# Kernel optimization log

Measured on AMD Instinct MI355X. Metric: run time of the kernel, lower is better.

The kernel has to match this reference:

```python
import jax, jax.numpy as jnp
import numpy as np

N = 4096          # leng_doc (number of tokens)
D_S = 70          # DEP_EMB_DIM + 2*BI_LSTM_PHASE_1_OUTPUT_DIM = 10 + 60

def setup_inputs() -> dict:
    key = jax.random.key(0)
    k1, k2 = jax.random.split(key)
    adj = jax.random.uniform(k1, (N, N, 2), dtype=jnp.float32)   # unweighted adjacency, 2 edge directions/channels
    s = jax.random.normal(k2, (N, D_S), dtype=jnp.float32)       # per-node edge-representation s
    return {"adj": adj, "s": s}

def reference(adj, s):
    # Faithful to CalculateHLayer-style math (CalculateSLayer analog):
    #   s_in[j,d]  = sum_i sum_k adj[i,j,k] * s[i,d]
    #   s_out[i,d] = sum_j sum_k adj[i,j,k] * s[j,d]
    # Sum over the channel axis k first, then contract the node axis with a GEMM
    # instead of materializing the (N,N,2,D) broadcast intermediate.
    a = adj.sum(axis=2)                 # (N, N)
    s_in = jnp.einsum('ij,id->jd', a, s)   # reduce over source nodes -> (N, D)
    s_out = jnp.einsum('ij,jd->id', a, s)  # reduce over target nodes -> (N, D)
    return (s_in, s_out)
```

## Files before the change

kernel.cpp:

```cpp
#include <hip/hip_runtime.h>


#define N    4096
#define D    70
#define DP   80
#define TILE 128
#define NT_D 5
#define NPART 32
#define ATP  132

typedef short short8  __attribute__((ext_vector_type(8)));
typedef short short4v __attribute__((ext_vector_type(4)));
typedef float f32x4   __attribute__((ext_vector_type(4)));

__device__ __forceinline__ unsigned short f2bf(float f) {
    unsigned u = __builtin_bit_cast(unsigned, f);
    u += 0x7FFFu + ((u >> 16) & 1u);
    return (unsigned short)(u >> 16);
}
__device__ __forceinline__ float bf2f(unsigned short h) {
    unsigned u = (unsigned)h << 16;
    return __builtin_bit_cast(float, u);
}
__device__ __forceinline__ short8 ld_b64x2(const unsigned short* p) {
    short4v lo = *(const short4v*)p;
    short4v hi = *(const short4v*)(p + 4);
    return __builtin_shufflevector(lo, hi, 0, 1, 2, 3, 4, 5, 6, 7);
}

__global__ __launch_bounds__(256) void build_sT(const float* __restrict__ s,
                                                unsigned short* __restrict__ sT) {
    __shared__ unsigned short tile[DP][264];
    const int t  = threadIdx.x;
    const int n0 = blockIdx.x * 256;
    #pragma unroll
    for (int d = 0; d < D; ++d)
        tile[d][t] = f2bf(s[(size_t)(n0 + t) * D + d]);
    __syncthreads();
    #pragma unroll
    for (int d = 0; d < DP; ++d) {
        unsigned short v = (d < D) ? tile[d][t] : (unsigned short)0;
        sT[(size_t)d * N + n0 + t] = v;
    }
}

template<bool USE_WS>
__global__ __launch_bounds__(512, 4) void fused_slayer(
    const float* __restrict__ adj,
    const unsigned short* __restrict__ sT,
    void* __restrict__ p_in_,
    void* __restrict__ p_out_)
{
    unsigned short* wi = (unsigned short*)p_in_;
    unsigned short* wo = (unsigned short*)p_out_;
    float* oi = (float*)p_in_;
    float* oo = (float*)p_out_;

    __shared__ __align__(16) unsigned short a_row[TILE][40];
    __shared__ __align__(16) unsigned short aTt[32][ATP];
    __shared__ __align__(16) unsigned short sTi[DP][136];
    __shared__ __align__(16) unsigned short sTj[DP][136];

    const int t    = threadIdx.x;
    const int lane = t & 63;
    const int w    = t >> 6;
    const int l16  = lane & 15;
    const int q    = lane >> 4;

    const int I0 = blockIdx.y * TILE;
    const int J0 = blockIdx.x * TILE;

    {
        const int c  = t & 15;
        const int rr = t >> 4;
        #pragma unroll
        for (int p = 0; p < 3; ++p) {
            int d = rr + 32 * p;
            if (d < DP) {
                uint4 vi = *(const uint4*)(sT + (size_t)d * N + I0 + 8 * c);
                uint4 vj = *(const uint4*)(sT + (size_t)d * N + J0 + 8 * c);
                *(uint4*)&sTi[d][8 * c] = vi;
                *(uint4*)&sTj[d][8 * c] = vj;
            }
        }
    }

    const f32x4 zero = {0.0f, 0.0f, 0.0f, 0.0f};
    f32x4 acc1[NT_D];
    #pragma unroll
    for (int nt = 0; nt < NT_D; ++nt) acc1[nt] = zero;

    const int slot_mt = w & 1;
    const int slot_nt = w >> 1;
    const bool extra  = (w < 2);

    const int jp = t & 15;
    const int ir = t >> 4;

    float4 v[4];
    #pragma unroll
    for (int it = 0; it < 4; ++it) {
        int i = 32 * it + ir;
        v[it] = *(const float4*)(adj + (size_t)(I0 + i) * (2 * N)
                                     + (size_t)(J0 + 2 * jp) * 2);
    }

    #pragma unroll
    for (int jc = 0; jc < 4; ++jc) {
        __syncthreads();

        #pragma unroll
        for (int it = 0; it < 4; ++it) {
            int i = 32 * it + ir;
            unsigned short b0 = f2bf(v[it].x + v[it].y);
            unsigned short b1 = f2bf(v[it].z + v[it].w);
            *(unsigned int*)&a_row[i][2 * jp] =
                (unsigned int)b0 | ((unsigned int)b1 << 16);
            aTt[2 * jp][i]     = b0;
            aTt[2 * jp + 1][i] = b1;
        }
        __syncthreads();

        if (jc < 3) {
            #pragma unroll
            for (int it = 0; it < 4; ++it) {
                int i = 32 * it + ir;
                v[it] = *(const float4*)(adj + (size_t)(I0 + i) * (2 * N)
                                             + (size_t)(J0 + 32 * (jc + 1) + 2 * jp) * 2);
            }
        }

        {
            short8 af = *(const short8*)&a_row[16 * w + l16][8 * q];
            #pragma unroll
            for (int nt = 0; nt < NT_D; ++nt) {
                short8 bf = *(const short8*)&sTj[16 * nt + l16][32 * jc + 8 * q];
                acc1[nt] = __builtin_amdgcn_mfma_f32_16x16x32_bf16(af, bf, acc1[nt], 0, 0, 0);
            }
        }

        {
            f32x4 acc2 = zero;
            #pragma unroll
            for (int ks = 0; ks < 4; ++ks) {
                short8 af = ld_b64x2(&aTt[16 * slot_mt + l16][32 * ks + 8 * q]);
                short8 bf = *(const short8*)&sTi[16 * slot_nt + l16][32 * ks + 8 * q];
                acc2 = __builtin_amdgcn_mfma_f32_16x16x32_bf16(af, bf, acc2, 0, 0, 0);
            }
            int d = 16 * slot_nt + l16;
            #pragma unroll
            for (int r = 0; r < 4; ++r) {
                int gj = J0 + 32 * jc + 16 * slot_mt + 4 * q + r;
                if (USE_WS) {
                    wi[((size_t)blockIdx.y * N + gj) * DP + d] = f2bf(acc2[r]);
                } else if (d < D) {
                    atomicAdd(&oi[(size_t)gj * D + d], acc2[r]);
                }
            }
            if (extra) {
                f32x4 acc3 = zero;
                #pragma unroll
                for (int ks = 0; ks < 4; ++ks) {
                    short8 af = ld_b64x2(&aTt[16 * w + l16][32 * ks + 8 * q]);
                    short8 bf = *(const short8*)&sTi[64 + l16][32 * ks + 8 * q];
                    acc3 = __builtin_amdgcn_mfma_f32_16x16x32_bf16(af, bf, acc3, 0, 0, 0);
                }
                int d2 = 64 + l16;
                #pragma unroll
                for (int r = 0; r < 4; ++r) {
                    int gj = J0 + 32 * jc + 16 * w + 4 * q + r;
                    if (USE_WS) {
                        wi[((size_t)blockIdx.y * N + gj) * DP + d2] = f2bf(acc3[r]);
                    } else if (d2 < D) {
                        atomicAdd(&oi[(size_t)gj * D + d2], acc3[r]);
                    }
                }
            }
        }
    }

    #pragma unroll
    for (int nt = 0; nt < NT_D; ++nt) {
        int d = 16 * nt + l16;
        #pragma unroll
        for (int r = 0; r < 4; ++r) {
            int gi = I0 + 16 * w + 4 * q + r;
            if (USE_WS) {
                wo[((size_t)blockIdx.x * N + gi) * DP + d] = f2bf(acc1[nt][r]);
            } else if (d < D) {
                atomicAdd(&oo[(size_t)gi * D + d], acc1[nt][r]);
            }
        }
    }
}

__global__ __launch_bounds__(128) void reduce_partials(
    const unsigned short* __restrict__ ws, float* __restrict__ out) {
    const int idx   = blockIdx.x * 128 + threadIdx.x;
    const int which = idx / (N * (DP / 8));
    const int rem   = idx % (N * (DP / 8));
    const int j     = rem / (DP / 8);
    const int g     = rem % (DP / 8);

    const unsigned short* base = ws + (size_t)which * ((size_t)NPART * N * DP)
                                    + (size_t)j * DP + 8 * g;
    float acc[8];
    #pragma unroll
    for (int e = 0; e < 8; ++e) acc[e] = 0.0f;
    #pragma unroll 8
    for (int p = 0; p < NPART; ++p) {
        short8 v = *(const short8*)(base + (size_t)p * N * DP);
        #pragma unroll
        for (int e = 0; e < 8; ++e)
            acc[e] += bf2f((unsigned short)v[e]);
    }

    float* o = out + (size_t)which * (N * D) + (size_t)j * D;
    #pragma unroll
    for (int e = 0; e < 8; ++e) {
        int d = 8 * g + e;
        if (d < D) o[d] = acc[e];
    }
}

extern "C" void kernel_launch(void* const* d_in, const int* in_sizes, int n_in,
                              void* d_out, int out_size, void* d_ws, size_t ws_size,
                              hipStream_t stream) {
    const float* adj = (const float*)d_in[0];
    const float* s   = (const float*)d_in[1];
    float* out = (float*)d_out;

    unsigned short* sT = (unsigned short*)d_ws;
    const size_t ST_BYTES = (size_t)DP * N * sizeof(unsigned short);
    unsigned short* ws_part = (unsigned short*)((char*)d_ws + ST_BYTES);
    const size_t PART_ELEMS = (size_t)NPART * N * DP;
    const size_t NEED = ST_BYTES + 2 * PART_ELEMS * sizeof(unsigned short);

    build_sT<<<dim3(N / 256), dim3(256), 0, stream>>>(s, sT);

    if (ws_size >= NEED) {
        fused_slayer<true><<<dim3(N / TILE, N / TILE), dim3(512), 0, stream>>>(
            adj, sT, ws_part , ws_part + PART_ELEMS );
        reduce_partials<<<dim3(2 * N * (DP / 8) / 128), dim3(128), 0, stream>>>(
            ws_part, out);
    } else {
        hipMemsetAsync(d_out, 0, (size_t)2 * N * D * sizeof(float), stream);
        fused_slayer<false><<<dim3(N / TILE, N / TILE), dim3(512), 0, stream>>>(
            adj, sT, out , out + (size_t)N * D );
    }
}
```

Before: 212.1 us.

## Fuse partial reduction into main kernel via last-block counters, double-buffer adjacency tiles

```diff
diff --git a/kernel.cpp b/kernel.cpp
--- a/kernel.cpp
+++ b/kernel.cpp
@@ -8,6 +8,7 @@
 #define NT_D 5
 #define NPART 32
 #define ATP  132
+#define SJP  136
 
 typedef short short8  __attribute__((ext_vector_type(8)));
 typedef short short4v __attribute__((ext_vector_type(4)));
@@ -48,51 +49,56 @@
 __global__ __launch_bounds__(512, 4) void fused_slayer(
     const float* __restrict__ adj,
     const unsigned short* __restrict__ sT,
-    void* __restrict__ p_in_,
-    void* __restrict__ p_out_)
+    unsigned short* __restrict__ wsi,
+    unsigned short* __restrict__ wso,
+    unsigned int*   __restrict__ cnt,
+    float* __restrict__ out)
 {
-    unsigned short* wi = (unsigned short*)p_in_;
-    unsigned short* wo = (unsigned short*)p_out_;
-    float* oi = (float*)p_in_;
-    float* oo = (float*)p_out_;
-
-    __shared__ __align__(16) unsigned short a_row[TILE][40];
-    __shared__ __align__(16) unsigned short aTt[32][ATP];
-    __shared__ __align__(16) unsigned short sTi[DP][136];
-    __shared__ __align__(16) unsigned short sTj[DP][136];
+    __shared__ __align__(16) unsigned short a_row[2][TILE][40];
+    __shared__ __align__(16) unsigned short aTt[2][32][ATP];
+    __shared__ __align__(16) unsigned short sTj[DP][SJP];
+    __shared__ int flag_in, flag_out;
 
     const int t    = threadIdx.x;
     const int lane = t & 63;
     const int w    = t >> 6;
     const int l16  = lane & 15;
     const int q    = lane >> 4;
-
-    const int I0 = blockIdx.y * TILE;
-    const int J0 = blockIdx.x * TILE;
-
-    {
-        const int c  = t & 15;
-        const int rr = t >> 4;
-        #pragma unroll
-        for (int p = 0; p < 3; ++p) {
-            int d = rr + 32 * p;
-            if (d < DP) {
-                uint4 vi = *(const uint4*)(sT + (size_t)d * N + I0 + 8 * c);
-                uint4 vj = *(const uint4*)(sT + (size_t)d * N + J0 + 8 * c);
-                *(uint4*)&sTi[d][8 * c] = vi;
-                *(uint4*)&sTj[d][8 * c] = vj;
-            }
-        }
-    }
-
-    const f32x4 zero = {0.0f, 0.0f, 0.0f, 0.0f};
-    f32x4 acc1[NT_D];
-    #pragma unroll
-    for (int nt = 0; nt < NT_D; ++nt) acc1[nt] = zero;
+    const int bx   = blockIdx.x;
+    const int by   = blockIdx.y;
+    const int I0   = by * TILE;
+    const int J0   = bx * TILE;
+
+    #pragma unroll
+    for (int p = 0; p < 3; ++p) {
+        int ii = t + 512 * p;
+        if (ii < DP * 16) {
+            int d = ii >> 4, c = ii & 15;
+            *(uint4*)&sTj[d][8 * c] = *(const uint4*)(sT + (size_t)d * N + J0 + 8 * c);
+        }
+    }
 
     const int slot_mt = w & 1;
     const int slot_nt = w >> 1;
     const bool extra  = (w < 2);
+    short8 bfi[4], bfe[4];
+    {
+        const int d = 16 * slot_nt + l16;
+        #pragma unroll
+        for (int ks = 0; ks < 4; ++ks)
+            bfi[ks] = *(const short8*)(sT + (size_t)d * N + I0 + 32 * ks + 8 * q);
+        if (extra) {
+            const int d2 = 64 + l16;
+            #pragma unroll
+            for (int ks = 0; ks < 4; ++ks)
+                bfe[ks] = *(const short8*)(sT + (size_t)d2 * N + I0 + 32 * ks + 8 * q);
+        }
+    }
+
+    const f32x4 zero = {0.0f, 0.0f, 0.0f, 0.0f};
+    f32x4 acc1[NT_D];
+    #pragma unroll
+    for (int nt = 0; nt < NT_D; ++nt) acc1[nt] = zero;
 
     const int jp = t & 15;
     const int ir = t >> 4;
@@ -107,17 +113,17 @@
 
     #pragma unroll
     for (int jc = 0; jc < 4; ++jc) {
-        __syncthreads();
+        const int b = jc & 1;
 
         #pragma unroll
         for (int it = 0; it < 4; ++it) {
             int i = 32 * it + ir;
             unsigned short b0 = f2bf(v[it].x + v[it].y);
             unsigned short b1 = f2bf(v[it].z + v[it].w);
-            *(unsigned int*)&a_row[i][2 * jp] =
+            *(unsigned int*)&a_row[b][i][2 * jp] =
                 (unsigned int)b0 | ((unsigned int)b1 << 16);
-            aTt[2 * jp][i]     = b0;
-            aTt[2 * jp + 1][i] = b1;
+            aTt[b][2 * jp][i]     = b0;
+            aTt[b][2 * jp + 1][i] = b1;
         }
         __syncthreads();
 
@@ -131,7 +137,7 @@
         }
 
         {
-            short8 af = *(const short8*)&a_row[16 * w + l16][8 * q];
+            short8 af = *(const short8*)&a_row[b][16 * w + l16][8 * q];
             #pragma unroll
             for (int nt = 0; nt < NT_D; ++nt) {
                 short8 bf = *(const short8*)&sTj[16 * nt + l16][32 * jc + 8 * q];
@@ -143,36 +149,34 @@
             f32x4 acc2 = zero;
             #pragma unroll
             for (int ks = 0; ks < 4; ++ks) {
-                short8 af = ld_b64x2(&aTt[16 * slot_mt + l16][32 * ks + 8 * q]);
-                short8 bf = *(const short8*)&sTi[16 * slot_nt + l16][32 * ks + 8 * q];
-                acc2 = __builtin_amdgcn_mfma_f32_16x16x32_bf16(af, bf, acc2, 0, 0, 0);
-            }
-            int d = 16 * slot_nt + l16;
+                short8 af2 = ld_b64x2(&aTt[b][16 * slot_mt + l16][32 * ks + 8 * q]);
+                acc2 = __builtin_amdgcn_mfma_f32_16x16x32_bf16(af2, bfi[ks], acc2, 0, 0, 0);
+            }
+            const int d = 16 * slot_nt + l16;
             #pragma unroll
             for (int r = 0; r < 4; ++r) {
                 int gj = J0 + 32 * jc + 16 * slot_mt + 4 * q + r;
                 if (USE_WS) {
-                    wi[((size_t)blockIdx.y * N + gj) * DP + d] = f2bf(acc2[r]);
+                    wsi[((size_t)by * N + gj) * DP + d] = f2bf(acc2[r]);
                 } else if (d < D) {
-                    atomicAdd(&oi[(size_t)gj * D + d], acc2[r]);
+                    atomicAdd(&out[(size_t)gj * D + d], acc2[r]);
                 }
             }
             if (extra) {
                 f32x4 acc3 = zero;
                 #pragma unroll
                 for (int ks = 0; ks < 4; ++ks) {
-                    short8 af = ld_b64x2(&aTt[16 * w + l16][32 * ks + 8 * q]);
-                    short8 bf = *(const short8*)&sTi[64 + l16][32 * ks + 8 * q];
-                    acc3 = __builtin_amdgcn_mfma_f32_16x16x32_bf16(af, bf, acc3, 0, 0, 0);
+                    short8 af3 = ld_b64x2(&aTt[b][16 * w + l16][32 * ks + 8 * q]);
+                    acc3 = __builtin_amdgcn_mfma_f32_16x16x32_bf16(af3, bfe[ks], acc3, 0, 0, 0);
                 }
-                int d2 = 64 + l16;
+                const int d2 = 64 + l16;
                 #pragma unroll
                 for (int r = 0; r < 4; ++r) {
                     int gj = J0 + 32 * jc + 16 * w + 4 * q + r;
                     if (USE_WS) {
-                        wi[((size_t)blockIdx.y * N + gj) * DP + d2] = f2bf(acc3[r]);
+                        wsi[((size_t)by * N + gj) * DP + d2] = f2bf(acc3[r]);
                     } else if (d2 < D) {
-                        atomicAdd(&oi[(size_t)gj * D + d2], acc3[r]);
+                        atomicAdd(&out[(size_t)gj * D + d2], acc3[r]);
                     }
                 }
             }
@@ -181,45 +185,71 @@
 
     #pragma unroll
     for (int nt = 0; nt < NT_D; ++nt) {
-        int d = 16 * nt + l16;
+        const int d = 16 * nt + l16;
         #pragma unroll
         for (int r = 0; r < 4; ++r) {
             int gi = I0 + 16 * w + 4 * q + r;
             if (USE_WS) {
-                wo[((size_t)blockIdx.x * N + gi) * DP + d] = f2bf(acc1[nt][r]);
+                wso[((size_t)bx * N + gi) * DP + d] = f2bf(acc1[nt][r]);
             } else if (d < D) {
-                atomicAdd(&oo[(size_t)gi * D + d], acc1[nt][r]);
-            }
-        }
-    }
-}
-
-__global__ __launch_bounds__(128) void reduce_partials(
-    const unsigned short* __restrict__ ws, float* __restrict__ out) {
-    const int idx   = blockIdx.x * 128 + threadIdx.x;
-    const int which = idx / (N * (DP / 8));
-    const int rem   = idx % (N * (DP / 8));
-    const int j     = rem / (DP / 8);
-    const int g     = rem % (DP / 8);
-
-    const unsigned short* base = ws + (size_t)which * ((size_t)NPART * N * DP)
-                                    + (size_t)j * DP + 8 * g;
-    float acc[8];
-    #pragma unroll
-    for (int e = 0; e < 8; ++e) acc[e] = 0.0f;
-    #pragma unroll 8
-    for (int p = 0; p < NPART; ++p) {
-        short8 v = *(const short8*)(base + (size_t)p * N * DP);
-        #pragma unroll
-        for (int e = 0; e < 8; ++e)
-            acc[e] += bf2f((unsigned short)v[e]);
-    }
-
-    float* o = out + (size_t)which * (N * D) + (size_t)j * D;
-    #pragma unroll
-    for (int e = 0; e < 8; ++e) {
-        int d = 8 * g + e;
-        if (d < D) o[d] = acc[e];
+                atomicAdd(&out[(size_t)N * D + (size_t)gi * D + d], acc1[nt][r]);
+            }
+        }
+    }
+
+    if (!USE_WS) return;
+
+    __threadfence();
+    __syncthreads();
+    if (t == 0) {
+        flag_in  = (atomicAdd(&cnt[bx],      1u) == NPART - 1);
+        flag_out = (atomicAdd(&cnt[32 + by], 1u) == NPART - 1);
+    }
+    __syncthreads();
+
+    if (flag_in) {
+        __threadfence();
+        for (int task = t; task < TILE * (DP / 8); task += 512) {
+            const int jl = task / (DP / 8);
+            const int g  = task % (DP / 8);
+            const int gj = J0 + jl;
+            float acc[8];
+            #pragma unroll
+            for (int e = 0; e < 8; ++e) acc[e] = 0.0f;
+            #pragma unroll 8
+            for (int p = 0; p < NPART; ++p) {
+                short8 vv = *(const short8*)(wsi + ((size_t)p * N + gj) * DP + 8 * g);
+                #pragma unroll
+                for (int e = 0; e < 8; ++e) acc[e] += bf2f((unsigned short)vv[e]);
+            }
+            #pragma unroll
+            for (int e = 0; e < 8; ++e) {
+                int d = 8 * g + e;
+                if (d < D) out[(size_t)gj * D + d] = acc[e];
+            }
+        }
+    }
+    if (flag_out) {
+        __threadfence();
+        for (int task = t; task < TILE * (DP / 8); task += 512) {
+            const int il = task / (DP / 8);
+            const int g  = task % (DP / 8);
+            const int gi = I0 + il;
+            float acc[8];
+            #pragma unroll
+            for (int e = 0; e < 8; ++e) acc[e] = 0.0f;
+            #pragma unroll 8
+            for (int p = 0; p < NPART; ++p) {
+                short8 vv = *(const short8*)(wso + ((size_t)p * N + gi) * DP + 8 * g);
+                #pragma unroll
+                for (int e = 0; e < 8; ++e) acc[e] += bf2f((unsigned short)vv[e]);
+            }
+            #pragma unroll
+            for (int e = 0; e < 8; ++e) {
+                int d = 8 * g + e;
+                if (d < D) out[(size_t)N * D + (size_t)gi * D + d] = acc[e];
+            }
+        }
     }
 }
 
@@ -231,21 +261,22 @@
     float* out = (float*)d_out;
 
     unsigned short* sT = (unsigned short*)d_ws;
-    const size_t ST_BYTES = (size_t)DP * N * sizeof(unsigned short);
-    unsigned short* ws_part = (unsigned short*)((char*)d_ws + ST_BYTES);
+    const size_t ST_BYTES   = (size_t)DP * N * sizeof(unsigned short);
+    unsigned int*   cnt     = (unsigned int*)((char*)d_ws + ST_BYTES);
+    unsigned short* ws_part = (unsigned short*)((char*)d_ws + ST_BYTES + 256);
     const size_t PART_ELEMS = (size_t)NPART * N * DP;
-    const size_t NEED = ST_BYTES + 2 * PART_ELEMS * sizeof(unsigned short);
+    const size_t NEED = ST_BYTES + 256
+                      + 2 * PART_ELEMS * sizeof(unsigned short);
 
     build_sT<<<dim3(N / 256), dim3(256), 0, stream>>>(s, sT);
 
     if (ws_size >= NEED) {
+        hipMemsetAsync(cnt, 0, 256, stream);
         fused_slayer<true><<<dim3(N / TILE, N / TILE), dim3(512), 0, stream>>>(
-            adj, sT, ws_part , ws_part + PART_ELEMS );
-        reduce_partials<<<dim3(2 * N * (DP / 8) / 128), dim3(128), 0, stream>>>(
-            ws_part, out);
+            adj, sT, ws_part, ws_part + PART_ELEMS, cnt, out);
     } else {
         hipMemsetAsync(d_out, 0, (size_t)2 * N * D * sizeof(float), stream);
         fused_slayer<false><<<dim3(N / TILE, N / TILE), dim3(512), 0, stream>>>(
-            adj, sT, out , out + (size_t)N * D );
-    }
-}
+            adj, sT, nullptr, nullptr, nullptr, out);
+    }
+}
```

New measurement: 664.2 us. +213.1%, slower.
